# Kernel optimization log

Hardware: AMD Instinct MI355X
Metric: run time of the kernel (lower is better)

## Reference

```python
import jax, jax.numpy as jnp
import numpy as np

N_AQI = 35
N_MEO = 18
H = N_AQI + 3 * N_MEO  # 89
T = 120
B = 32768


def setup_inputs() -> dict:
    key = jax.random.key(0)
    ks = jax.random.split(key, 9)
    s = 1.0 / np.sqrt(H)
    return {
        "out": jax.random.normal(ks[0], (B, T, H), dtype=jnp.float32),
        # GRUCell params (PyTorch layout: [3H, in], gate order r,z,n)
        "W_ih": jax.random.normal(ks[1], (3 * H, H), dtype=jnp.float32) * s,
        "W_hh": jax.random.normal(ks[2], (3 * H, H), dtype=jnp.float32) * s,
        "b_ih": jax.random.normal(ks[3], (3 * H,), dtype=jnp.float32) * s,
        "b_hh": jax.random.normal(ks[4], (3 * H,), dtype=jnp.float32) * s,
        # metric_fc: 89 -> 32
        "W_m": jax.random.normal(ks[5], (32, H), dtype=jnp.float32) * s,
        "b_m": jax.random.normal(ks[6], (32,), dtype=jnp.float32) * s,
        # output_fc: 32 -> 1
        "W_o": jax.random.normal(ks[7], (1, 32), dtype=jnp.float32) * (1.0 / np.sqrt(32)),
        "b_o": jax.random.normal(ks[8], (1,), dtype=jnp.float32) * (1.0 / np.sqrt(32)),
    }


def reference(out, W_ih, W_hh, b_ih, b_hh, W_m, b_m, W_o, b_o):
    h0 = jnp.zeros((out.shape[0], H), dtype=out.dtype)
    xs = jnp.transpose(out[:, :T, :], (1, 0, 2))  # (T, B, H)

    def step(h, x):
        gi = x @ W_ih.T + b_ih          # (B, 3H)
        gh = h @ W_hh.T + b_hh          # (B, 3H)
        i_r, i_z, i_n = jnp.split(gi, 3, axis=-1)
        h_r, h_z, h_n = jnp.split(gh, 3, axis=-1)
        r = jax.nn.sigmoid(i_r + h_r)
        z = jax.nn.sigmoid(i_z + h_z)
        n = jnp.tanh(i_n + r * h_n)
        h_new = (1.0 - z) * n + z * h   # PyTorch GRUCell update
        return h_new, None

    h, _ = jax.lax.scan(step, h0, xs)
    out_mmetric = jax.nn.sigmoid(h @ W_m.T + b_m)        # (B, 32)
    out_mscore = jax.nn.sigmoid(out_mmetric @ W_o.T + b_o)  # (B, 1)
    return out_mscore, out_mmetric
```

## Files before the change

kernel.cpp:

```cpp
#include <hip/hip_runtime.h>
#include <hip/hip_bf16.h>

#define Hn    89
#define Tn    120
#define BM    64
#define XPF   100
#define XPB   (XPF*4)
#define XPLANE (BM*XPB)
#define HPB   208
#define HPLANE (BM*HPB)
#define ROWB  (Tn*Hn*4)
#define TSTEP (Hn*4)
#define OMAX  ((unsigned)(BM*ROWB - 16))

#define SRZ (-1.44269504f)
#define SNN ( 2.88539008f)

using bf16   = __bf16;
using bf16x4 = __attribute__((ext_vector_type(4))) __bf16;
using bf16x8 = __attribute__((ext_vector_type(8))) __bf16;
typedef __attribute__((ext_vector_type(4))) float f32x4;

typedef const __attribute__((address_space(1))) unsigned int guint;
typedef __attribute__((address_space(3))) unsigned int luint;

__device__ __forceinline__ f32x4 ld4(const float* p) {
  f32x4 v; __builtin_memcpy(&v, p, 16); return v;
}
__device__ __forceinline__ bf16x8 pack8(f32x4 a, f32x4 b) {
  bf16x8 r;
  r[0]=(bf16)a[0]; r[1]=(bf16)a[1]; r[2]=(bf16)a[2]; r[3]=(bf16)a[3];
  r[4]=(bf16)b[0]; r[5]=(bf16)b[1]; r[6]=(bf16)b[2]; r[7]=(bf16)b[3];
  return r;
}
__device__ __forceinline__ float frcp(float x) { return __builtin_amdgcn_rcpf(x); }
__device__ __forceinline__ float fex2(float x) { return __builtin_amdgcn_exp2f(x); }
__device__ __forceinline__ float fsig(float x) { return frcp(1.f + fex2(-1.44269504f * x)); }

__global__ __launch_bounds__(512, 4)
void gru_fused(const float* __restrict__ X,
               const float* __restrict__ Wih,
               const float* __restrict__ Whh,
               const float* __restrict__ bih,
               const float* __restrict__ bhh,
               const float* __restrict__ Wm,
               const float* __restrict__ bm,
               const float* __restrict__ Wo,
               const float* __restrict__ bo,
               float* __restrict__ Y,
               int Bt)
{
  __shared__ __align__(16) char lds[2 * XPLANE + 2 * HPLANE];
  char* const XF0 = lds;
  char* const HL0 = lds + 2 * XPLANE;

  const int tid  = threadIdx.x;
  const int lane = tid & 63;
  const int wv   = tid >> 6;
  const int l15  = lane & 15;
  const int kg   = lane >> 4;
  const bool cmp = (wv < 6);
  const size_t brow0 = (size_t)blockIdx.x * BM;
  const char* xgw = (const char*)(X + brow0 * (size_t)(Tn * Hn));

  bf16x8 Bf[3][2][3];
  float binq[4] = {0.f, 0.f, 0.f, 0.f};
  if (cmp) {
    const int jA = wv * 16 + l15;
    const bool jAok = (jA < Hn);
#pragma unroll
    for (int g = 0; g < 3; ++g)
#pragma unroll
      for (int s = 0; s < 2; ++s) {
        const float* W = s ? Whh : Wih;
        const float sc = (g < 2) ? SRZ : SNN;
#pragma unroll
        for (int kt = 0; kt < 3; ++kt) {
          bf16x8 f;
          const int k0 = kt * 32 + kg * 8;
#pragma unroll
          for (int e = 0; e < 8; ++e) {
            const int k = k0 + e;
            float v = 0.f;
            if (jAok) {
              if (k < Hn) v = sc * W[(size_t)(g * Hn + jA) * Hn + k];
              else if (k == Hn && s == 1)
                v = (g < 2) ? sc * (bih[g * Hn + jA] + bhh[g * Hn + jA])
                            : SNN * bhh[2 * Hn + jA];
            }
            f[e] = (bf16)v;
          }
          Bf[g][s][kt] = f;
        }
      }
#pragma unroll
    for (int q = 0; q < 4; ++q) {
      const int j = wv * 16 + kg * 4 + q;
      binq[q] = (j < Hn) ? SNN * bih[2 * Hn + j] : 0.f;
    }
  }

  const unsigned cb   = (wv == 6) ? 0u : 3328u;
  const int     nch   = (wv == 6) ? 13 : 12;
  const unsigned dstb = cb * 4u;

  auto stage = [&](char* dst, unsigned toff) {
    unsigned l4 = (unsigned)lane * 4u;
    asm volatile("" : "+v"(l4));
#pragma unroll
    for (int m = 0; m < 13; ++m) {
      if (m < nch) {
        const unsigned idx4 = cb + (unsigned)(m * 256) + l4;
        const unsigned r = idx4 / 100u;
        const unsigned c = idx4 - r * 100u;
        unsigned o = r * (unsigned)ROWB + (c << 2) + toff;
        if (o > OMAX) o = OMAX;
        __builtin_amdgcn_global_load_lds(
            (guint*)(xgw + o), (luint*)(dst + dstb + (unsigned)(m * 1024)), 16, 0, 0);
      }
    }
    asm volatile("s_waitcnt vmcnt(0)" ::: "memory");
    if (wv == 7 && lane == 63) {
      const float x88 = *(const float*)(xgw + 63u * (unsigned)ROWB + 352u + toff);
      *(float*)(dst + 63 * XPB + 352) = x88;
    }
  };

  const unsigned xro = (unsigned)(l15 * XPB + kg * 32);
  const unsigned hro = (unsigned)(l15 * HPB + kg * 16);
  const unsigned hwo = (unsigned)(l15 * HPB + (wv * 16 + kg * 4) * 2);

  if (cmp) {
    bf16x4 z4 = {(bf16)0.f, (bf16)0.f, (bf16)0.f, (bf16)0.f};
    if (wv == 5 && kg == 2) z4[1] = (bf16)1.0f;
#pragma unroll
    for (int mt = 0; mt < 4; ++mt)
      *(bf16x4*)(HL0 + hwo + mt * 16 * HPB) = z4;
  } else {
    stage(XF0, 0);
  }

  unsigned tof = TSTEP;
  for (int t = 0; t < Tn; ++t) {
    const int b = t & 1;
    __syncthreads();

    if (cmp) {
      __builtin_amdgcn_s_setprio(1);
      const char* xr = XF0 + b * XPLANE + xro;
      const char* hr = HL0 + b * HPLANE + hro;
      const char* hp = HL0 + b * HPLANE + hwo;
      char*       hw = HL0 + (b ^ 1) * HPLANE + hwo;
#pragma unroll
      for (int mt = 0; mt < 4; ++mt) {
        f32x4 ar = {0,0,0,0}, az = {0,0,0,0}, ain = {0,0,0,0}, ahn = {0,0,0,0};
#pragma unroll
        for (int kt = 0; kt < 3; ++kt) {
          const f32x4 xa = *(const f32x4*)(xr + mt * (16 * XPB) + kt * 128);
          const f32x4 xb = *(const f32x4*)(xr + mt * (16 * XPB) + kt * 128 + 16);
          const bf16x8 xf = pack8(xa, xb);
          const bf16x8 hf = *(const bf16x8*)(hr + mt * (16 * HPB) + kt * 64);
          ar  = __builtin_amdgcn_mfma_f32_16x16x32_bf16(Bf[0][0][kt], xf, ar, 0, 0, 0);
          ar  = __builtin_amdgcn_mfma_f32_16x16x32_bf16(Bf[0][1][kt], hf, ar, 0, 0, 0);
          az  = __builtin_amdgcn_mfma_f32_16x16x32_bf16(Bf[1][0][kt], xf, az, 0, 0, 0);
          az  = __builtin_amdgcn_mfma_f32_16x16x32_bf16(Bf[1][1][kt], hf, az, 0, 0, 0);
          ain = __builtin_amdgcn_mfma_f32_16x16x32_bf16(Bf[2][0][kt], xf, ain, 0, 0, 0);
          ahn = __builtin_amdgcn_mfma_f32_16x16x32_bf16(Bf[2][1][kt], hf, ahn, 0, 0, 0);
        }
        const bf16x4 hp4 = *(const bf16x4*)(hp + mt * (16 * HPB));
        bf16x4 wv4;
#pragma unroll
        for (int q = 0; q < 4; ++q) {
          const float r_ = frcp(1.f + fex2(ar[q]));
          const float z_ = frcp(1.f + fex2(az[q]));
          const float s_ = ain[q] + binq[q] + r_ * ahn[q];
          const float n_ = fmaf(-2.f, frcp(1.f + fex2(s_)), 1.f);
          const float hv = n_ + z_ * ((float)hp4[q] - n_);
          wv4[q] = (bf16)hv;
        }
        if (wv == 5) {
          if (kg == 2) { wv4[1] = (bf16)1.0f; wv4[2] = (bf16)0.f; wv4[3] = (bf16)0.f; }
          if (kg == 3) { wv4[0] = (bf16)0.f; wv4[1] = (bf16)0.f;
                         wv4[2] = (bf16)0.f; wv4[3] = (bf16)0.f; }
        }
        *(bf16x4*)(hw + mt * (16 * HPB)) = wv4;
      }
      __builtin_amdgcn_s_setprio(0);
    } else {
      if (t + 1 < Tn) { stage(XF0 + (b ^ 1) * XPLANE, tof); tof += TSTEP; }
    }
  }
  __syncthreads();

  char* const mlb = XF0;
  for (int p = tid; p < BM * 32; p += 512) {
    const int r = p >> 5, c = p & 31;
    const char* hr2 = HL0 + r * HPB;
    const float* wrow = Wm + c * Hn;
    float acc = bm[c];
#pragma unroll 4
    for (int cbk = 0; cbk < 11; ++cbk) {
      const bf16x8 hv = *(const bf16x8*)(hr2 + cbk * 16);
      const f32x4 wa = ld4(wrow + cbk * 8);
      const f32x4 wb = ld4(wrow + cbk * 8 + 4);
      acc = fmaf((float)hv[0], wa[0], acc); acc = fmaf((float)hv[1], wa[1], acc);
      acc = fmaf((float)hv[2], wa[2], acc); acc = fmaf((float)hv[3], wa[3], acc);
      acc = fmaf((float)hv[4], wb[0], acc); acc = fmaf((float)hv[5], wb[1], acc);
      acc = fmaf((float)hv[6], wb[2], acc); acc = fmaf((float)hv[7], wb[3], acc);
    }
    acc = fmaf((float)*(const bf16*)(hr2 + 176), wrow[88], acc);
    const float mv = fsig(acc);
    *(float*)(mlb + r * 128 + c * 4) = mv;
    Y[(size_t)Bt + (brow0 + r) * 32 + c] = mv;
  }
  __syncthreads();
  if (tid < BM) {
    float acc = bo[0];
#pragma unroll
    for (int c = 0; c < 32; ++c)
      acc = fmaf(*(const float*)(mlb + tid * 128 + c * 4), Wo[c], acc);
    Y[brow0 + tid] = fsig(acc);
  }
}

extern "C" void kernel_launch(void* const* d_in, const int* in_sizes, int n_in,
                              void* d_out, int out_size, void* d_ws, size_t ws_size,
                              hipStream_t stream) {
  const float* X   = (const float*)d_in[0];
  const float* Wih = (const float*)d_in[1];
  const float* Whh = (const float*)d_in[2];
  const float* bih = (const float*)d_in[3];
  const float* bhh = (const float*)d_in[4];
  const float* Wm  = (const float*)d_in[5];
  const float* bm  = (const float*)d_in[6];
  const float* Wo  = (const float*)d_in[7];
  const float* bo  = (const float*)d_in[8];

  const int B = in_sizes[0] / (Tn * Hn);
  dim3 grid(B / BM), block(512);
  gru_fused<<<grid, block, 0, stream>>>(X, Wih, Whh, bih, bhh, Wm, bm, Wo, bo,
                                        (float*)d_out, B);
}
```

Baseline: 626.4 us.

## Load x directly from global in compute waves, drop LDS staging producers

Removes the producer waves that staged x into LDS with global_load_lds. Every wave now loads its x fragments straight from global memory into registers. The block grows to 128 rows with 12 waves arranged as 6 j-tiles by 2 row halves. The third K-tile of W_ih is reindexed so it reads overlapping columns 57..88 and zeroes the duplicates, which avoids out-of-bounds reads. This trades explicit double-buffered prefetch for more waves and larger LDS freed for h, and it risks exposing global load latency on each timestep's critical path.

```diff
diff --git a/kernel.cpp b/kernel.cpp
--- a/kernel.cpp
+++ b/kernel.cpp
@@ -1,17 +1,13 @@
 #include <hip/hip_runtime.h>
 #include <hip/hip_bf16.h>
 
-#define Hn    89
-#define Tn    120
-#define BM    64
-#define XPF   100
-#define XPB   (XPF*4)
-#define XPLANE (BM*XPB)
-#define HPB   208
+#define Hn   89
+#define Tn   120
+#define BM   128
+#define HPB  208
 #define HPLANE (BM*HPB)
-#define ROWB  (Tn*Hn*4)
+#define ROWB (Tn*Hn*4)
 #define TSTEP (Hn*4)
-#define OMAX  ((unsigned)(BM*ROWB - 16))
 
 #define SRZ (-1.44269504f)
 #define SNN ( 2.88539008f)
@@ -21,10 +17,7 @@
 using bf16x8 = __attribute__((ext_vector_type(8))) __bf16;
 typedef __attribute__((ext_vector_type(4))) float f32x4;
 
-typedef const __attribute__((address_space(1))) unsigned int guint;
-typedef __attribute__((address_space(3))) unsigned int luint;
-
-__device__ __forceinline__ f32x4 ld4(const float* p) {
+__device__ __forceinline__ f32x4 ld4(const void* p) {
   f32x4 v; __builtin_memcpy(&v, p, 16); return v;
 }
 __device__ __forceinline__ bf16x8 pack8(f32x4 a, f32x4 b) {
@@ -37,7 +30,7 @@
 __device__ __forceinline__ float fex2(float x) { return __builtin_amdgcn_exp2f(x); }
 __device__ __forceinline__ float fsig(float x) { return frcp(1.f + fex2(-1.44269504f * x)); }
 
-__global__ __launch_bounds__(512, 4)
+__global__ __launch_bounds__(768, 3)
 void gru_fused(const float* __restrict__ X,
                const float* __restrict__ Wih,
                const float* __restrict__ Whh,
@@ -50,152 +43,129 @@
                float* __restrict__ Y,
                int Bt)
 {
-  __shared__ __align__(16) char lds[2 * XPLANE + 2 * HPLANE];
-  char* const XF0 = lds;
-  char* const HL0 = lds + 2 * XPLANE;
+  __shared__ __align__(16) char hraw[2 * HPLANE];
 
   const int tid  = threadIdx.x;
   const int lane = tid & 63;
   const int wv   = tid >> 6;
+  const int jt   = wv >> 1;
+  const int hf   = wv & 1;
   const int l15  = lane & 15;
   const int kg   = lane >> 4;
-  const bool cmp = (wv < 6);
   const size_t brow0 = (size_t)blockIdx.x * BM;
   const char* xgw = (const char*)(X + brow0 * (size_t)(Tn * Hn));
 
+  const int jA = jt * 16 + l15;
+  const bool jAok = (jA < Hn);
   bf16x8 Bf[3][2][3];
-  float binq[4] = {0.f, 0.f, 0.f, 0.f};
-  if (cmp) {
-    const int jA = wv * 16 + l15;
-    const bool jAok = (jA < Hn);
-#pragma unroll
-    for (int g = 0; g < 3; ++g)
-#pragma unroll
-      for (int s = 0; s < 2; ++s) {
-        const float* W = s ? Whh : Wih;
-        const float sc = (g < 2) ? SRZ : SNN;
-#pragma unroll
-        for (int kt = 0; kt < 3; ++kt) {
-          bf16x8 f;
-          const int k0 = kt * 32 + kg * 8;
-#pragma unroll
-          for (int e = 0; e < 8; ++e) {
-            const int k = k0 + e;
-            float v = 0.f;
-            if (jAok) {
-              if (k < Hn) v = sc * W[(size_t)(g * Hn + jA) * Hn + k];
-              else if (k == Hn && s == 1)
+#pragma unroll
+  for (int g = 0; g < 3; ++g)
+#pragma unroll
+    for (int s = 0; s < 2; ++s) {
+      const float sc = (g < 2) ? SRZ : SNN;
+#pragma unroll
+      for (int kt = 0; kt < 3; ++kt) {
+        bf16x8 f;
+#pragma unroll
+        for (int e = 0; e < 8; ++e) {
+          float v = 0.f;
+          if (jAok) {
+            if (s == 0) {
+              const int k = (kt < 2) ? kt * 32 + kg * 8 + e : 57 + kg * 8 + e;
+              if (kt < 2 || k >= 64)
+                v = sc * Wih[(size_t)(g * Hn + jA) * Hn + k];
+            } else {
+              const int k = kt * 32 + kg * 8 + e;
+              if (k < Hn)       v = sc * Whh[(size_t)(g * Hn + jA) * Hn + k];
+              else if (k == Hn)
                 v = (g < 2) ? sc * (bih[g * Hn + jA] + bhh[g * Hn + jA])
                             : SNN * bhh[2 * Hn + jA];
             }
-            f[e] = (bf16)v;
           }
-          Bf[g][s][kt] = f;
+          f[e] = (bf16)v;
         }
-      }
-#pragma unroll
-    for (int q = 0; q < 4; ++q) {
-      const int j = wv * 16 + kg * 4 + q;
-      binq[q] = (j < Hn) ? SNN * bih[2 * Hn + j] : 0.f;
+        Bf[g][s][kt] = f;
+      }
     }
-  }
-
-  const unsigned cb   = (wv == 6) ? 0u : 3328u;
-  const int     nch   = (wv == 6) ? 13 : 12;
-  const unsigned dstb = cb * 4u;
-
-  auto stage = [&](char* dst, unsigned toff) {
-    unsigned l4 = (unsigned)lane * 4u;
-    asm volatile("" : "+v"(l4));
-#pragma unroll
-    for (int m = 0; m < 13; ++m) {
-      if (m < nch) {
-        const unsigned idx4 = cb + (unsigned)(m * 256) + l4;
-        const unsigned r = idx4 / 100u;
-        const unsigned c = idx4 - r * 100u;
-        unsigned o = r * (unsigned)ROWB + (c << 2) + toff;
-        if (o > OMAX) o = OMAX;
-        __builtin_amdgcn_global_load_lds(
-            (guint*)(xgw + o), (luint*)(dst + dstb + (unsigned)(m * 1024)), 16, 0, 0);
-      }
-    }
-    asm volatile("s_waitcnt vmcnt(0)" ::: "memory");
-    if (wv == 7 && lane == 63) {
-      const float x88 = *(const float*)(xgw + 63u * (unsigned)ROWB + 352u + toff);
-      *(float*)(dst + 63 * XPB + 352) = x88;
-    }
-  };
-
-  const unsigned xro = (unsigned)(l15 * XPB + kg * 32);
-  const unsigned hro = (unsigned)(l15 * HPB + kg * 16);
-  const unsigned hwo = (unsigned)(l15 * HPB + (wv * 16 + kg * 4) * 2);
-
-  if (cmp) {
+
+  float binq[4];
+#pragma unroll
+  for (int q = 0; q < 4; ++q) {
+    const int j = jt * 16 + kg * 4 + q;
+    binq[q] = (j < Hn) ? SNN * bih[2 * Hn + j] : 0.f;
+  }
+
+  unsigned rb[4];
+#pragma unroll
+  for (int mt = 0; mt < 4; ++mt)
+    rb[mt] = (unsigned)((hf * 64 + mt * 16 + l15) * ROWB);
+  const unsigned ko[3] = { (unsigned)(kg * 32),
+                           (unsigned)(128 + kg * 32),
+                           (unsigned)(228 + kg * 32) };
+  const unsigned hro = (unsigned)((hf * 64 + l15) * HPB + kg * 16);
+  const unsigned hco = (unsigned)((hf * 64 + l15) * HPB + (jt * 16 + kg * 4) * 2);
+
+  {
     bf16x4 z4 = {(bf16)0.f, (bf16)0.f, (bf16)0.f, (bf16)0.f};
-    if (wv == 5 && kg == 2) z4[1] = (bf16)1.0f;
+    if (jt == 5 && kg == 2) z4[1] = (bf16)1.0f;
 #pragma unroll
     for (int mt = 0; mt < 4; ++mt)
-      *(bf16x4*)(HL0 + hwo + mt * 16 * HPB) = z4;
-  } else {
-    stage(XF0, 0);
-  }
-
-  unsigned tof = TSTEP;
+      *(bf16x4*)(hraw + hco + mt * 16 * HPB) = z4;
+  }
+
   for (int t = 0; t < Tn; ++t) {
     const int b = t & 1;
     __syncthreads();
-
-    if (cmp) {
-      __builtin_amdgcn_s_setprio(1);
-      const char* xr = XF0 + b * XPLANE + xro;
-      const char* hr = HL0 + b * HPLANE + hro;
-      const char* hp = HL0 + b * HPLANE + hwo;
-      char*       hw = HL0 + (b ^ 1) * HPLANE + hwo;
-#pragma unroll
-      for (int mt = 0; mt < 4; ++mt) {
-        f32x4 ar = {0,0,0,0}, az = {0,0,0,0}, ain = {0,0,0,0}, ahn = {0,0,0,0};
-#pragma unroll
-        for (int kt = 0; kt < 3; ++kt) {
-          const f32x4 xa = *(const f32x4*)(xr + mt * (16 * XPB) + kt * 128);
-          const f32x4 xb = *(const f32x4*)(xr + mt * (16 * XPB) + kt * 128 + 16);
-          const bf16x8 xf = pack8(xa, xb);
-          const bf16x8 hf = *(const bf16x8*)(hr + mt * (16 * HPB) + kt * 64);
-          ar  = __builtin_amdgcn_mfma_f32_16x16x32_bf16(Bf[0][0][kt], xf, ar, 0, 0, 0);
-          ar  = __builtin_amdgcn_mfma_f32_16x16x32_bf16(Bf[0][1][kt], hf, ar, 0, 0, 0);
-          az  = __builtin_amdgcn_mfma_f32_16x16x32_bf16(Bf[1][0][kt], xf, az, 0, 0, 0);
-          az  = __builtin_amdgcn_mfma_f32_16x16x32_bf16(Bf[1][1][kt], hf, az, 0, 0, 0);
-          ain = __builtin_amdgcn_mfma_f32_16x16x32_bf16(Bf[2][0][kt], xf, ain, 0, 0, 0);
-          ahn = __builtin_amdgcn_mfma_f32_16x16x32_bf16(Bf[2][1][kt], hf, ahn, 0, 0, 0);
-        }
-        const bf16x4 hp4 = *(const bf16x4*)(hp + mt * (16 * HPB));
-        bf16x4 wv4;
-#pragma unroll
-        for (int q = 0; q < 4; ++q) {
-          const float r_ = frcp(1.f + fex2(ar[q]));
-          const float z_ = frcp(1.f + fex2(az[q]));
-          const float s_ = ain[q] + binq[q] + r_ * ahn[q];
-          const float n_ = fmaf(-2.f, frcp(1.f + fex2(s_)), 1.f);
-          const float hv = n_ + z_ * ((float)hp4[q] - n_);
-          wv4[q] = (bf16)hv;
-        }
-        if (wv == 5) {
-          if (kg == 2) { wv4[1] = (bf16)1.0f; wv4[2] = (bf16)0.f; wv4[3] = (bf16)0.f; }
-          if (kg == 3) { wv4[0] = (bf16)0.f; wv4[1] = (bf16)0.f;
-                         wv4[2] = (bf16)0.f; wv4[3] = (bf16)0.f; }
-        }
-        *(bf16x4*)(hw + mt * (16 * HPB)) = wv4;
-      }
-      __builtin_amdgcn_s_setprio(0);
-    } else {
-      if (t + 1 < Tn) { stage(XF0 + (b ^ 1) * XPLANE, tof); tof += TSTEP; }
+    const char* hrp = hraw + b * HPLANE;
+    char*       hwp = hraw + (b ^ 1) * HPLANE;
+    const unsigned xb = (unsigned)t * (unsigned)TSTEP;
+
+    __builtin_amdgcn_s_setprio(1);
+#pragma unroll
+    for (int mt = 0; mt < 4; ++mt) {
+      bf16x8 xf[3], hfr[3];
+#pragma unroll
+      for (int kt = 0; kt < 3; ++kt) {
+        const char* pa = xgw + (rb[mt] + xb + ko[kt]);
+        xf[kt]  = pack8(ld4(pa), ld4(pa + 16));
+        hfr[kt] = *(const bf16x8*)(hrp + hro + mt * 16 * HPB + kt * 64);
+      }
+      f32x4 ar = {0,0,0,0}, az = {0,0,0,0}, ain = {0,0,0,0}, ahn = {0,0,0,0};
+#pragma unroll
+      for (int kt = 0; kt < 3; ++kt) {
+        ar  = __builtin_amdgcn_mfma_f32_16x16x32_bf16(Bf[0][0][kt], xf[kt],  ar, 0, 0, 0);
+        ar  = __builtin_amdgcn_mfma_f32_16x16x32_bf16(Bf[0][1][kt], hfr[kt], ar, 0, 0, 0);
+        az  = __builtin_amdgcn_mfma_f32_16x16x32_bf16(Bf[1][0][kt], xf[kt],  az, 0, 0, 0);
+        az  = __builtin_amdgcn_mfma_f32_16x16x32_bf16(Bf[1][1][kt], hfr[kt], az, 0, 0, 0);
+        ain = __builtin_amdgcn_mfma_f32_16x16x32_bf16(Bf[2][0][kt], xf[kt],  ain, 0, 0, 0);
+        ahn = __builtin_amdgcn_mfma_f32_16x16x32_bf16(Bf[2][1][kt], hfr[kt], ahn, 0, 0, 0);
+      }
+      const bf16x4 hp4 = *(const bf16x4*)(hrp + hco + mt * 16 * HPB);
+      bf16x4 wv4;
+#pragma unroll
+      for (int q = 0; q < 4; ++q) {
+        const float r_ = frcp(1.f + fex2(ar[q]));
+        const float z_ = frcp(1.f + fex2(az[q]));
+        const float s_ = ain[q] + binq[q] + r_ * ahn[q];
+        const float n_ = fmaf(-2.f, frcp(1.f + fex2(s_)), 1.f);
+        const float hv = n_ + z_ * ((float)hp4[q] - n_);
+        wv4[q] = (bf16)hv;
+      }
+      if (jt == 5) {
+        if (kg == 2) { wv4[1] = (bf16)1.0f; wv4[2] = (bf16)0.f; wv4[3] = (bf16)0.f; }
+        if (kg == 3) { wv4[0] = (bf16)0.f; wv4[1] = (bf16)0.f;
+                       wv4[2] = (bf16)0.f; wv4[3] = (bf16)0.f; }
+      }
+      *(bf16x4*)(hwp + hco + mt * 16 * HPB) = wv4;
     }
+    __builtin_amdgcn_s_setprio(0);
   }
   __syncthreads();
 
-  char* const mlb = XF0;
-  for (int p = tid; p < BM * 32; p += 512) {
+  char* const mlb = hraw + HPLANE;
+  for (int p = tid; p < BM * 32; p += 768) {
     const int r = p >> 5, c = p & 31;
-    const char* hr2 = HL0 + r * HPB;
+    const char* hr2 = hraw + r * HPB;
     const float* wrow = Wm + c * Hn;
     float acc = bm[c];
 #pragma unroll 4
@@ -237,7 +207,7 @@
   const float* bo  = (const float*)d_in[8];
 
   const int B = in_sizes[0] / (Tn * Hn);
-  dim3 grid(B / BM), block(512);
+  dim3 grid(B / BM), block(768);
   gru_fused<<<grid, block, 0, stream>>>(X, Wih, Whh, bih, bhh, Wm, bm, Wo, bo,
                                         (float*)d_out, B);
 }
```

Measured after the change: 898.1 us. 1.43x slower.
